# Performance work log

Hardware: AMD Instinct MI355X
Metric: run time of the kernel (lower is better)

The kernel has to match this reference:

```python
import jax, jax.numpy as jnp
import numpy as np

HIDDEN = 1024
INTER = 4096

def setup_inputs() -> dict:
    key = jax.random.key(0)
    k1, k2, k3, k4, k5 = jax.random.split(key, 5)
    hidden_states = jax.random.normal(k1, (4, 2048, HIDDEN), dtype=jnp.float32)
    # Linear params: W stored pre-transposed as [in, out], matching W = dense.weight.t()
    W1 = jax.random.normal(k2, (HIDDEN, INTER), dtype=jnp.float32) * (1.0 / np.sqrt(HIDDEN))
    b1 = jax.random.normal(k3, (INTER,), dtype=jnp.float32) * 0.02
    W2 = jax.random.normal(k4, (INTER, HIDDEN), dtype=jnp.float32) * (1.0 / np.sqrt(INTER))
    b2 = jax.random.normal(k5, (HIDDEN,), dtype=jnp.float32) * 0.02
    return {"hidden_states": hidden_states, "W1": W1, "b1": b1, "W2": W2, "b2": b2}

def reference(hidden_states, W1, b1, W2, b2):
    # Tiled loops in the original are exactly a dense 2-layer MLP with ReLU.
    h = jax.nn.relu(jnp.einsum('bsh,hi->bsi', hidden_states, W1) + b1)
    return jnp.einsum('bsi,ih->bsh', h, W2) + b2
```

## Files before the change

kernel.cpp:

```cpp
#include <hip/hip_runtime.h>
#include <cstddef>

typedef short short8 __attribute__((ext_vector_type(8)));
typedef unsigned short ushort8 __attribute__((ext_vector_type(8)));
typedef float f32x4 __attribute__((ext_vector_type(4)));

#define AS1(p) ((const __attribute__((address_space(1))) void*)(p))
#define AS3(p) ((__attribute__((address_space(3))) void*)(p))

__device__ __forceinline__ unsigned short f2bf(float f) {
  unsigned int u = __builtin_bit_cast(unsigned int, f);
  u += 0x7FFFu + ((u >> 16) & 1u);
  return (unsigned short)(u >> 16);
}

__device__ __forceinline__ void gload_lds16(const void* g, void* l) {
  __builtin_amdgcn_global_load_lds(AS1(g), AS3(l), 16, 0, 0);
}

__global__ __launch_bounds__(256)
void prep_fused(const float* __restrict__ X,
                const float* __restrict__ W1,
                const float* __restrict__ W2,
                unsigned short* __restrict__ Xbf,
                unsigned short* __restrict__ W1t,
                unsigned short* __restrict__ W2t) {
  const int b   = blockIdx.x;
  const int tid = threadIdx.x;

  if (b >= 8192) {
    const size_t i = (size_t)(b - 8192) * 256 + tid;
    float4 v = *reinterpret_cast<const float4*>(X + i * 4);
    ushort4 o;
    o.x = f2bf(v.x); o.y = f2bf(v.y); o.z = f2bf(v.z); o.w = f2bf(v.w);
    *reinterpret_cast<ushort4*>(Xbf + i * 4) = o;
    return;
  }

  __shared__ float tile[32][33];
  const float* in;
  unsigned short* out;
  int Kd, Nd, n0, k0;
  if (b < 4096) {
    in = W1; out = W1t; Kd = 1024; Nd = 4096;
    n0 = (b & 127) * 32;
    k0 = (b >> 7) * 32;
  } else {
    const int b2 = b - 4096;
    in = W2; out = W2t; Kd = 4096; Nd = 1024;
    n0 = (b2 & 31) * 32;
    k0 = (b2 >> 5) * 32;
  }
  const int tx = tid & 31;
  const int ty = tid >> 5;
#pragma unroll
  for (int i = 0; i < 4; ++i)
    tile[ty + i * 8][tx] = in[(size_t)(k0 + ty + i * 8) * Nd + n0 + tx];
  __syncthreads();
#pragma unroll
  for (int i = 0; i < 4; ++i)
    out[(size_t)(n0 + ty + i * 8) * Kd + k0 + tx] = f2bf(tile[tx][ty + i * 8]);
}

__global__ void cvt_f32_bf16(const float* __restrict__ in,
                             unsigned short* __restrict__ out, int n4) {
  int i = blockIdx.x * blockDim.x + threadIdx.x;
  if (i >= n4) return;
  float4 v = *reinterpret_cast<const float4*>(in + (size_t)i * 4);
  ushort4 o;
  o.x = f2bf(v.x); o.y = f2bf(v.y); o.z = f2bf(v.z); o.w = f2bf(v.w);
  *reinterpret_cast<ushort4*>(out + (size_t)i * 4) = o;
}

__global__ void transpose_cvt(const float* __restrict__ in,
                              unsigned short* __restrict__ out,
                              int Kd, int Nd) {
  __shared__ float tile[32][33];
  const int n0 = blockIdx.x * 32;
  const int k0 = blockIdx.y * 32;
  const int tx = threadIdx.x;
  const int ty = threadIdx.y;
#pragma unroll
  for (int i = 0; i < 4; ++i)
    tile[ty + i * 8][tx] = in[(size_t)(k0 + ty + i * 8) * Nd + n0 + tx];
  __syncthreads();
#pragma unroll
  for (int i = 0; i < 4; ++i)
    out[(size_t)(n0 + ty + i * 8) * Kd + k0 + tx] = f2bf(tile[tx][ty + i * 8]);
}

#define PH(ABUF, BBUF, H, KK, STAGE, WAITC)                                    \
  {                                                                            \
    if ((H) == 0) {                                                            \
      _Pragma("unroll")                                                        \
      for (int ni = 0; ni < NB; ++ni)                                          \
        bfr[ni] = *reinterpret_cast<const short8*>((BBUF) + bread[ni][KK]);    \
    }                                                                          \
    short8 afr[4];                                                             \
    _Pragma("unroll")                                                          \
    for (int m2 = 0; m2 < 4; ++m2)                                             \
      afr[m2] = *reinterpret_cast<const short8*>((ABUF) + aread[(H)*4+m2][KK]);\
    STAGE;                                                                     \
    __builtin_amdgcn_s_barrier();                                              \
    asm volatile("s_waitcnt lgkmcnt(0)" ::: "memory");                         \
    __builtin_amdgcn_sched_barrier(0);                                         \
    __builtin_amdgcn_s_setprio(1);                                             \
    _Pragma("unroll")                                                          \
    for (int m2 = 0; m2 < 4; ++m2) {                                           \
      _Pragma("unroll")                                                        \
      for (int ni = 0; ni < NB; ++ni)                                          \
        acc[(H)*4+m2][ni] = __builtin_amdgcn_mfma_f32_16x16x32_bf16(           \
            afr[m2], bfr[ni], acc[(H)*4+m2][ni], 0, 0, 0);                     \
    }                                                                          \
    __builtin_amdgcn_s_setprio(0);                                             \
    WAITC;                                                                     \
    __builtin_amdgcn_s_barrier();                                              \
  }

template <int BN, int RELU_BF16_OUT>
__global__ __launch_bounds__(512, 2)
void gemm8p(const unsigned short* __restrict__ A, int lda,
            const unsigned short* __restrict__ Bp, int ldb,
            const float* __restrict__ bias,
            void* __restrict__ C, int ldc, int K, int nbx) {
  constexpr int PWN     = BN / 4;
  constexpr int NB      = PWN / 16;
  constexpr int LOADS_B = BN / 128;
  constexpr int BHROWS  = BN / 2;
  constexpr int BHSZ    = BHROWS * 128;
  extern __shared__ char lds[];
  char* const A0b = lds;
  char* const A1b = lds + 32768;
  char* const B0b = lds + 65536;
  char* const B1b = lds + 65536 + 2 * BHSZ;

  const int tid  = threadIdx.x;
  const int lane = tid & 63;
  const int wid  = tid >> 6;
  const int wm   = wid >> 2;
  const int wn   = wid & 3;

  const int cpx     = gridDim.x >> 3;
  const int logical = (blockIdx.x & 7) * cpx + (blockIdx.x >> 3);
  const int bx = logical % nbx;
  const int by = logical / nbx;
  const int m0 = by * 256;
  const int n0 = bx * BN;

  f32x4 acc[8][NB];
#pragma unroll
  for (int i = 0; i < 8; ++i)
#pragma unroll
    for (int j = 0; j < NB; ++j)
      acc[i][j] = (f32x4){0.f, 0.f, 0.f, 0.f};

  size_t aofs0, aofs1, bofs0, bofs1 = 0;
  {
    int sr = tid * 16, nat = sr ^ (((sr >> 7) & 7) << 4);
    aofs0 = (size_t)(m0 + (nat >> 7)) * lda + ((nat & 127) >> 1);
    bofs0 = (size_t)(n0 + (nat >> 7)) * ldb + ((nat & 127) >> 1);
    sr = (512 + tid) * 16; nat = sr ^ (((sr >> 7) & 7) << 4);
    aofs1 = (size_t)(m0 + (nat >> 7)) * lda + ((nat & 127) >> 1);
    if (LOADS_B == 2)
      bofs1 = (size_t)(n0 + (nat >> 7)) * ldb + ((nat & 127) >> 1);
  }
  const int dst0 = (tid & 448) * 16;
  const int dst1 = dst0 + 8192;

  auto stA = [&](char* ab, int half, int kel) {
    gload_lds16(A + aofs0 + (size_t)half * 128 * lda + kel, ab + half * 16384 + dst0);
    gload_lds16(A + aofs1 + (size_t)half * 128 * lda + kel, ab + half * 16384 + dst1);
  };
  auto stB = [&](char* bb, int half, int kel) {
    gload_lds16(Bp + bofs0 + (size_t)half * BHROWS * ldb + kel, bb + half * BHSZ + dst0);
    if constexpr (LOADS_B == 2)
      gload_lds16(Bp + bofs1 + (size_t)half * BHROWS * ldb + kel, bb + half * BHSZ + dst1);
  };
  auto waitLB = [&]() {
    if constexpr (LOADS_B == 2) asm volatile("s_waitcnt vmcnt(2)" ::: "memory");
    else                        asm volatile("s_waitcnt vmcnt(1)" ::: "memory");
  };

  int aread[8][2], bread[NB][2];
#pragma unroll
  for (int mi = 0; mi < 8; ++mi)
#pragma unroll
    for (int kk = 0; kk < 2; ++kk) {
      int nat = (wm * 128 + mi * 16 + (lane & 15)) * 128 + kk * 64 + (lane >> 4) * 16;
      aread[mi][kk] = nat ^ (((nat >> 7) & 7) << 4);
    }
#pragma unroll
  for (int ni = 0; ni < NB; ++ni)
#pragma unroll
    for (int kk = 0; kk < 2; ++kk) {
      int nat = (wn * PWN + ni * 16 + (lane & 15)) * 128 + kk * 64 + (lane >> 4) * 16;
      bread[ni][kk] = nat ^ (((nat >> 7) & 7) << 4);
    }

  stB(B0b, 0, 0);
  stB(B0b, 1, 0);
  stA(A0b, 0, 0);
  stA(A0b, 1, 0);
  stB(B1b, 0, 64);
  waitLB();
  __builtin_amdgcn_s_barrier();

  const int niter = K >> 7;
  for (int it = 0; it < niter; ++it) {
    const bool last = (it == niter - 1);
    const int kb = it << 7;
    short8 bfr[NB];
    PH(A0b, B0b, 0, 0, stB(B1b, 1, kb + 64), ((void)0));
    PH(A0b, B0b, 1, 0, stA(A1b, 0, kb + 64), ((void)0));
    PH(A0b, B0b, 0, 1, stA(A1b, 1, kb + 64), ((void)0));
    PH(A0b, B0b, 1, 1, { if (!last) stB(B0b, 0, kb + 128); },
       { if (last) { asm volatile("s_waitcnt vmcnt(0)" ::: "memory"); } else waitLB(); });
    PH(A1b, B1b, 0, 0, { if (!last) stB(B0b, 1, kb + 128); }, ((void)0));
    PH(A1b, B1b, 1, 0, { if (!last) stA(A0b, 0, kb + 128); }, ((void)0));
    PH(A1b, B1b, 0, 1, { if (!last) stA(A0b, 1, kb + 128); }, ((void)0));
    PH(A1b, B1b, 1, 1, { if (!last) stB(B1b, 0, kb + 192); },
       { if (!last) waitLB(); });
  }

  const int row0 = m0 + wm * 128 + (lane >> 4) * 4;
  const int col0 = n0 + wn * PWN + (lane & 15);
#pragma unroll
  for (int ni = 0; ni < NB; ++ni) {
    const int c = col0 + ni * 16;
    const float bv = bias[c];
#pragma unroll
    for (int mi = 0; mi < 8; ++mi) {
#pragma unroll
      for (int r = 0; r < 4; ++r) {
        const size_t idx = (size_t)(row0 + mi * 16 + r) * ldc + c;
        float v = acc[mi][ni][r] + bv;
        if (RELU_BF16_OUT) {
          v = v > 0.f ? v : 0.f;
          ((unsigned short*)C)[idx] = f2bf(v);
        } else {
          ((float*)C)[idx] = v;
        }
      }
    }
  }
}

template <int A_F32, int RELU_BF16_OUT>
__global__ __launch_bounds__(256, 2)
void gemm_bf16(const void* __restrict__ Ap, int lda,
               const unsigned short* __restrict__ B, int ldb,
               const float* __restrict__ bias,
               void* __restrict__ C, int ldc,
               int K, int beta) {
  __shared__ char lds[32768];
  char* const As = lds;
  char* const Bs = lds + 16384;

  const int tid  = threadIdx.x;
  const int lane = tid & 63;
  const int w    = tid >> 6;
  const int wm   = w >> 1;
  const int wn   = w & 1;
  const int m0   = blockIdx.y * 128;
  const int n0   = blockIdx.x * 128;

  f32x4 acc[4][4];
#pragma unroll
  for (int i = 0; i < 4; ++i)
#pragma unroll
    for (int j = 0; j < 4; ++j)
      acc[i][j] = (f32x4){0.f, 0.f, 0.f, 0.f};

  int srow[4], scol[4], sbase[4];
#pragma unroll
  for (int j = 0; j < 4; ++j) {
    const int stored  = (j * 256 + tid) * 16;
    const int natural = stored ^ (((stored >> 7) & 7) << 4);
    srow[j]  = natural >> 7;
    scol[j]  = (natural & 127) >> 1;
    sbase[j] = (j * 256 + (tid & 192)) * 16;
  }

  size_t agofs[4];
  int ast[4];
  if (A_F32) {
#pragma unroll
    for (int pq = 0; pq < 4; ++pq) {
      const int idx = pq * 256 + tid;
      const int rr  = idx >> 3;
      const int kbe = (idx & 7) * 8;
      agofs[pq] = (size_t)(m0 + rr) * lda + kbe;
      const int nat = rr * 128 + kbe * 2;
      ast[pq] = nat ^ (((nat >> 7) & 7) << 4);
    }
  }

  const int nsteps = K >> 6;
  for (int ks = 0; ks < nsteps; ++ks) {
    const int k0 = ks << 6;
    if (A_F32) {
      const float* Af = (const float*)Ap;
#pragma unroll
      for (int pq = 0; pq < 4; ++pq) {
        const float* sp = Af + agofs[pq] + k0;
        float4 x0 = *reinterpret_cast<const float4*>(sp);
        float4 x1 = *reinterpret_cast<const float4*>(sp + 4);
        ushort8 v;
        v[0] = f2bf(x0.x); v[1] = f2bf(x0.y); v[2] = f2bf(x0.z); v[3] = f2bf(x0.w);
        v[4] = f2bf(x1.x); v[5] = f2bf(x1.y); v[6] = f2bf(x1.z); v[7] = f2bf(x1.w);
        *reinterpret_cast<ushort8*>(As + ast[pq]) = v;
      }
    } else {
      const unsigned short* Ab = (const unsigned short*)Ap;
#pragma unroll
      for (int j = 0; j < 4; ++j)
        gload_lds16(Ab + (size_t)(m0 + srow[j]) * lda + (k0 + scol[j]),
                    As + sbase[j]);
    }
#pragma unroll
    for (int j = 0; j < 4; ++j)
      gload_lds16(B + (size_t)(n0 + srow[j]) * ldb + (k0 + scol[j]),
                  Bs + sbase[j]);
    __syncthreads();

#pragma unroll
    for (int kk = 0; kk < 2; ++kk) {
      const int kb = kk * 64 + (lane >> 4) * 16;
      short8 af[4], bfv[4];
#pragma unroll
      for (int mi = 0; mi < 4; ++mi) {
        int nat = (wm * 64 + mi * 16 + (lane & 15)) * 128 + kb;
        int st  = nat ^ (((nat >> 7) & 7) << 4);
        af[mi] = *reinterpret_cast<const short8*>(As + st);
      }
#pragma unroll
      for (int ni = 0; ni < 4; ++ni) {
        int nat = (wn * 64 + ni * 16 + (lane & 15)) * 128 + kb;
        int st  = nat ^ (((nat >> 7) & 7) << 4);
        bfv[ni] = *reinterpret_cast<const short8*>(Bs + st);
      }
#pragma unroll
      for (int mi = 0; mi < 4; ++mi)
#pragma unroll
        for (int ni = 0; ni < 4; ++ni)
          acc[mi][ni] = __builtin_amdgcn_mfma_f32_16x16x32_bf16(
              af[mi], bfv[ni], acc[mi][ni], 0, 0, 0);
    }
    __syncthreads();
  }

  const int row0 = m0 + wm * 64 + (lane >> 4) * 4;
  const int col0 = n0 + wn * 64 + (lane & 15);
#pragma unroll
  for (int ni = 0; ni < 4; ++ni) {
    const int c = col0 + ni * 16;
    const float bv = beta ? 0.f : bias[c];
#pragma unroll
    for (int mi = 0; mi < 4; ++mi) {
#pragma unroll
      for (int rr = 0; rr < 4; ++rr) {
        const size_t idx = (size_t)(row0 + mi * 16 + rr) * ldc + c;
        float v = acc[mi][ni][rr] + bv;
        if (RELU_BF16_OUT) {
          v = v > 0.f ? v : 0.f;
          ((unsigned short*)C)[idx] = f2bf(v);
        } else {
          if (beta) v += ((float*)C)[idx];
          ((float*)C)[idx] = v;
        }
      }
    }
  }
}

extern "C" void kernel_launch(void* const* d_in, const int* in_sizes, int n_in,
                              void* d_out, int out_size, void* d_ws, size_t ws_size,
                              hipStream_t stream) {
  const float* X  = (const float*)d_in[0];
  const float* W1 = (const float*)d_in[1];
  const float* b1 = (const float*)d_in[2];
  const float* W2 = (const float*)d_in[3];
  const float* b2 = (const float*)d_in[4];
  float* out = (float*)d_out;

  const int M = 8192, H = 1024, I = 4096;
  const size_t MB = 1024 * 1024;

  char* ws = (char*)d_ws;
  unsigned short* W1t = (unsigned short*)ws;
  unsigned short* W2t = (unsigned short*)(ws + 8 * MB);

  if (ws_size >= 80 * MB) {
    unsigned short* Xbf = (unsigned short*)((char*)d_out + 16 * MB);
    unsigned short* Hbf = (unsigned short*)(ws + 16 * MB);
    prep_fused<<<16384, 256, 0, stream>>>(X, W1, W2, Xbf, W1t, W2t);
    gemm8p<256, 1><<<512, 512, 131072, stream>>>(Xbf, H, W1t, H, b1, Hbf, I, H, I / 256);
    gemm8p<128, 0><<<256, 512, 98304, stream>>>(Hbf, I, W2t, I, b2, out, H, I, H / 128);
    return;
  }

  transpose_cvt<<<dim3(I / 32, H / 32), dim3(32, 8), 0, stream>>>(W1, W1t, H, I);
  transpose_cvt<<<dim3(H / 32, I / 32), dim3(32, 8), 0, stream>>>(W2, W2t, I, H);

  int Ic, useXbf;
  unsigned short* Xbf = nullptr;
  unsigned short* Hc;
  if (ws_size >= 64 * MB) {
    Ic = 2048; useXbf = 1;
    Xbf = (unsigned short*)(ws + 16 * MB);
    Hc  = (unsigned short*)(ws + 32 * MB);
  } else if (ws_size >= 48 * MB) {
    Ic = 1024; useXbf = 1;
    Xbf = (unsigned short*)(ws + 16 * MB);
    Hc  = (unsigned short*)(ws + 32 * MB);
  } else if (ws_size >= 32 * MB) {
    Ic = 1024; useXbf = 0;
    Hc  = (unsigned short*)(ws + 16 * MB);
  } else if (ws_size >= 24 * MB) {
    Ic = 512;  useXbf = 0;
    Hc  = (unsigned short*)(ws + 16 * MB);
  } else if (ws_size >= 20 * MB) {
    Ic = 256;  useXbf = 0;
    Hc  = (unsigned short*)(ws + 16 * MB);
  } else {
    Ic = 128;  useXbf = 0;
    Hc  = (unsigned short*)(ws + 16 * MB);
  }

  if (useXbf) {
    int n4 = (M * H) / 4;
    cvt_f32_bf16<<<(n4 + 255) / 256, 256, 0, stream>>>(X, Xbf, n4);
  }

  const int nch = I / Ic;
  for (int c = 0; c < nch; ++c) {
    const int i0 = c * Ic;
    if (useXbf)
      gemm_bf16<0, 1><<<dim3(Ic / 128, M / 128), 256, 0, stream>>>(
          Xbf, H, W1t + (size_t)i0 * H, H, b1 + i0, Hc, Ic, H, 0);
    else
      gemm_bf16<1, 1><<<dim3(Ic / 128, M / 128), 256, 0, stream>>>(
          X, H, W1t + (size_t)i0 * H, H, b1 + i0, Hc, Ic, H, 0);
    gemm_bf16<0, 0><<<dim3(H / 128, M / 128), 256, 0, stream>>>(
        Hc, Ic, W2t + i0, I, b2, out, H, Ic, c > 0);
  }
}
```

Before: 161.7 us.

## Replace first GEMM with 256-thread 256x256-tile double-buffered bf16 MFMA kernel

Adds a new GEMM kernel, gemm_bw, for the first MLP layer. Each 4-wave workgroup computes a 256x256 tile with an 8x8 grid of 16x16x32 MFMA accumulators per wave. It uses double-buffered global-to-LDS loads into an XOR-swizzled layout and a simple vmcnt wait and barrier pipeline. It replaces the 512-thread gemm8p variant to cut per-wave LDS reads and scheduling overhead. The cost is very high register pressure (256 accumulator VGPRs) and a simpler pipeline with less fine-grained overlap.

```diff
diff --git a/kernel.cpp b/kernel.cpp
--- a/kernel.cpp
+++ b/kernel.cpp
@@ -16,6 +16,11 @@
 
 __device__ __forceinline__ void gload_lds16(const void* g, void* l) {
   __builtin_amdgcn_global_load_lds(AS1(g), AS3(l), 16, 0, 0);
+}
+
+template <int N>
+__device__ __forceinline__ void vwait() {
+  asm volatile("s_waitcnt vmcnt(%0)" :: "n"(N) : "memory");
 }
 
 __global__ __launch_bounds__(256)
@@ -87,6 +92,130 @@
 #pragma unroll
   for (int i = 0; i < 4; ++i)
     out[(size_t)(n0 + ty + i * 8) * Kd + k0 + tx] = f2bf(tile[tx][ty + i * 8]);
+}
+
+template <int RELU_BF16_OUT>
+__global__ __launch_bounds__(256, 1)
+void gemm_bw(const unsigned short* __restrict__ A, int lda,
+             const unsigned short* __restrict__ B, int ldb,
+             const float* __restrict__ bias,
+             void* __restrict__ C, int ldc, int K, int nbx) {
+  extern __shared__ char lds[];
+
+  const int tid  = threadIdx.x;
+  const int lane = tid & 63;
+  const int wid  = tid >> 6;
+  const int wm   = wid >> 1;
+  const int wn   = wid & 1;
+
+  const int cpx     = gridDim.x >> 3;
+  const int logical = (blockIdx.x & 7) * cpx + (blockIdx.x >> 3);
+  const int m0 = (logical / nbx) * 256;
+  const int n0 = (logical % nbx) * 256;
+
+  f32x4 acc[8][8];
+#pragma unroll
+  for (int i = 0; i < 8; ++i)
+#pragma unroll
+    for (int j = 0; j < 8; ++j)
+      acc[i][j] = (f32x4){0.f, 0.f, 0.f, 0.f};
+
+  size_t aofs[8], bofs[8];
+  int sb[8];
+#pragma unroll
+  for (int j = 0; j < 8; ++j) {
+    const int stored = (j * 256 + tid) * 16;
+    const int nat    = stored ^ (((stored >> 7) & 7) << 4);
+    const int row    = nat >> 7;
+    const int kel    = (nat & 127) >> 1;
+    aofs[j] = (size_t)(m0 + row) * lda + kel;
+    bofs[j] = (size_t)(n0 + row) * ldb + kel;
+    sb[j]   = j * 4096 + (tid & 192) * 16;
+  }
+
+  auto stage = [&](int d, int k0) {
+    char* ab = lds + d * 65536;
+    char* bb = ab + 32768;
+#pragma unroll
+    for (int j = 0; j < 8; ++j) gload_lds16(A + aofs[j] + k0, ab + sb[j]);
+#pragma unroll
+    for (int j = 0; j < 8; ++j) gload_lds16(B + bofs[j] + k0, bb + sb[j]);
+  };
+
+  int ard[8][2], brd[8][2];
+#pragma unroll
+  for (int mi = 0; mi < 8; ++mi)
+#pragma unroll
+    for (int kk = 0; kk < 2; ++kk) {
+      const int nat = (wm * 128 + mi * 16 + (lane & 15)) * 128 +
+                      kk * 64 + (lane >> 4) * 16;
+      ard[mi][kk] = nat ^ (((nat >> 7) & 7) << 4);
+    }
+#pragma unroll
+  for (int ni = 0; ni < 8; ++ni)
+#pragma unroll
+    for (int kk = 0; kk < 2; ++kk) {
+      const int nat = (wn * 128 + ni * 16 + (lane & 15)) * 128 +
+                      kk * 64 + (lane >> 4) * 16;
+      brd[ni][kk] = nat ^ (((nat >> 7) & 7) << 4);
+    }
+
+  stage(0, 0);
+
+  const int NT = K >> 6;
+  for (int t = 0; t < NT; ++t) {
+    const int cur = t & 1;
+    if (t + 1 < NT) {
+      stage(cur ^ 1, (t + 1) << 6);
+      vwait<16>();
+    } else {
+      vwait<0>();
+    }
+    __builtin_amdgcn_s_barrier();
+    __builtin_amdgcn_sched_barrier(0);
+
+    char* ab = lds + cur * 65536;
+    char* bb = ab + 32768;
+#pragma unroll
+    for (int kk = 0; kk < 2; ++kk) {
+      short8 bfv[8];
+#pragma unroll
+      for (int ni = 0; ni < 8; ++ni)
+        bfv[ni] = *reinterpret_cast<const short8*>(bb + brd[ni][kk]);
+#pragma unroll
+      for (int mi = 0; mi < 8; ++mi) {
+        const short8 af = *reinterpret_cast<const short8*>(ab + ard[mi][kk]);
+#pragma unroll
+        for (int ni = 0; ni < 8; ++ni)
+          acc[mi][ni] = __builtin_amdgcn_mfma_f32_16x16x32_bf16(
+              af, bfv[ni], acc[mi][ni], 0, 0, 0);
+      }
+    }
+    __builtin_amdgcn_sched_barrier(0);
+    __builtin_amdgcn_s_barrier();
+  }
+
+  const int row0 = m0 + wm * 128 + (lane >> 4) * 4;
+  const int col0 = n0 + wn * 128 + (lane & 15);
+#pragma unroll
+  for (int ni = 0; ni < 8; ++ni) {
+    const int c = col0 + ni * 16;
+    const float bv = bias[c];
+#pragma unroll
+    for (int mi = 0; mi < 8; ++mi) {
+#pragma unroll
+      for (int r = 0; r < 4; ++r) {
+        const size_t idx = (size_t)(row0 + mi * 16 + r) * ldc + c;
+        float v = acc[mi][ni][r] + bv;
+        if (RELU_BF16_OUT) {
+          v = v > 0.f ? v : 0.f;
+          ((unsigned short*)C)[idx] = f2bf(v);
+        } else {
+          ((float*)C)[idx] = v;
+        }
+      }
+    }
+  }
 }
 
 #define PH(ABUF, BBUF, H, KK, STAGE, WAITC)                                    \
@@ -394,8 +523,10 @@
     unsigned short* Xbf = (unsigned short*)((char*)d_out + 16 * MB);
     unsigned short* Hbf = (unsigned short*)(ws + 16 * MB);
     prep_fused<<<16384, 256, 0, stream>>>(X, W1, W2, Xbf, W1t, W2t);
-    gemm8p<256, 1><<<512, 512, 131072, stream>>>(Xbf, H, W1t, H, b1, Hbf, I, H, I / 256);
-    gemm8p<128, 0><<<256, 512, 98304, stream>>>(Hbf, I, W2t, I, b2, out, H, I, H / 128);
+    gemm_bw<1><<<512, 256, 131072, stream>>>(
+        Xbf, H, W1t, H, b1, Hbf, I, H, I / 256);
+    gemm8p<128, 0><<<256, 512, 98304, stream>>>(
+        Hbf, I, W2t, I, b2, out, H, I, H / 128);
     return;
   }
 
```

After: 211.3 us. 30.7% more time.

## Replace 8-phase interleaved GEMM pipeline with simple double-buffered K=64 loop

Applied to the files above, without the earlier changes.

Swaps the hand-scheduled 8-phase ping-pong GEMM, which interleaved partial A/B loads with MFMA groups and used setprio and sched barriers, for a plain double-buffered loop. Each step issues the whole next 64-wide K tile into the other LDS buffer, waits for the previous tile, and runs all MFMAs on it. This makes the schedule simpler and needs fewer barriers per step. It risks losing the fine-grained overlap and wave-priority tuning of the old pipeline.

```diff
diff --git a/kernel.cpp b/kernel.cpp
--- a/kernel.cpp
+++ b/kernel.cpp
@@ -16,6 +16,11 @@
 
 __device__ __forceinline__ void gload_lds16(const void* g, void* l) {
   __builtin_amdgcn_global_load_lds(AS1(g), AS3(l), 16, 0, 0);
+}
+
+template <int N>
+__device__ __forceinline__ void vwait() {
+  asm volatile("s_waitcnt vmcnt(%0)" :: "n"(N) : "memory");
 }
 
 __global__ __launch_bounds__(256)
@@ -89,50 +94,19 @@
     out[(size_t)(n0 + ty + i * 8) * Kd + k0 + tx] = f2bf(tile[tx][ty + i * 8]);
 }
 
-#define PH(ABUF, BBUF, H, KK, STAGE, WAITC)                                    \
-  {                                                                            \
-    if ((H) == 0) {                                                            \
-      _Pragma("unroll")                                                        \
-      for (int ni = 0; ni < NB; ++ni)                                          \
-        bfr[ni] = *reinterpret_cast<const short8*>((BBUF) + bread[ni][KK]);    \
-    }                                                                          \
-    short8 afr[4];                                                             \
-    _Pragma("unroll")                                                          \
-    for (int m2 = 0; m2 < 4; ++m2)                                             \
-      afr[m2] = *reinterpret_cast<const short8*>((ABUF) + aread[(H)*4+m2][KK]);\
-    STAGE;                                                                     \
-    __builtin_amdgcn_s_barrier();                                              \
-    asm volatile("s_waitcnt lgkmcnt(0)" ::: "memory");                         \
-    __builtin_amdgcn_sched_barrier(0);                                         \
-    __builtin_amdgcn_s_setprio(1);                                             \
-    _Pragma("unroll")                                                          \
-    for (int m2 = 0; m2 < 4; ++m2) {                                           \
-      _Pragma("unroll")                                                        \
-      for (int ni = 0; ni < NB; ++ni)                                          \
-        acc[(H)*4+m2][ni] = __builtin_amdgcn_mfma_f32_16x16x32_bf16(           \
-            afr[m2], bfr[ni], acc[(H)*4+m2][ni], 0, 0, 0);                     \
-    }                                                                          \
-    __builtin_amdgcn_s_setprio(0);                                             \
-    WAITC;                                                                     \
-    __builtin_amdgcn_s_barrier();                                              \
-  }
-
 template <int BN, int RELU_BF16_OUT>
 __global__ __launch_bounds__(512, 2)
-void gemm8p(const unsigned short* __restrict__ A, int lda,
-            const unsigned short* __restrict__ Bp, int ldb,
-            const float* __restrict__ bias,
-            void* __restrict__ C, int ldc, int K, int nbx) {
-  constexpr int PWN     = BN / 4;
-  constexpr int NB      = PWN / 16;
-  constexpr int LOADS_B = BN / 128;
-  constexpr int BHROWS  = BN / 2;
-  constexpr int BHSZ    = BHROWS * 128;
+void gemm_cf(const unsigned short* __restrict__ A, int lda,
+             const unsigned short* __restrict__ B, int ldb,
+             const float* __restrict__ bias,
+             void* __restrict__ C, int ldc, int K, int nbx) {
+  constexpr int PWN    = BN / 4;
+  constexpr int NB     = PWN / 16;
+  constexpr int AUNITS = 4;
+  constexpr int BUNITS = BN / 64;
+  constexpr int LPT    = AUNITS + BUNITS;
+  constexpr int BUFSZ  = 32768 + BN * 128;
   extern __shared__ char lds[];
-  char* const A0b = lds;
-  char* const A1b = lds + 32768;
-  char* const B0b = lds + 65536;
-  char* const B1b = lds + 65536 + 2 * BHSZ;
 
   const int tid  = threadIdx.x;
   const int lane = tid & 63;
@@ -142,10 +116,8 @@
 
   const int cpx     = gridDim.x >> 3;
   const int logical = (blockIdx.x & 7) * cpx + (blockIdx.x >> 3);
-  const int bx = logical % nbx;
-  const int by = logical / nbx;
-  const int m0 = by * 256;
-  const int n0 = bx * BN;
+  const int m0 = (logical / nbx) * 256;
+  const int n0 = (logical % nbx) * BN;
 
   f32x4 acc[8][NB];
 #pragma unroll
@@ -154,72 +126,80 @@
     for (int j = 0; j < NB; ++j)
       acc[i][j] = (f32x4){0.f, 0.f, 0.f, 0.f};
 
-  size_t aofs0, aofs1, bofs0, bofs1 = 0;
-  {
-    int sr = tid * 16, nat = sr ^ (((sr >> 7) & 7) << 4);
-    aofs0 = (size_t)(m0 + (nat >> 7)) * lda + ((nat & 127) >> 1);
-    bofs0 = (size_t)(n0 + (nat >> 7)) * ldb + ((nat & 127) >> 1);
-    sr = (512 + tid) * 16; nat = sr ^ (((sr >> 7) & 7) << 4);
-    aofs1 = (size_t)(m0 + (nat >> 7)) * lda + ((nat & 127) >> 1);
-    if (LOADS_B == 2)
-      bofs1 = (size_t)(n0 + (nat >> 7)) * ldb + ((nat & 127) >> 1);
-  }
-  const int dst0 = (tid & 448) * 16;
-  const int dst1 = dst0 + 8192;
-
-  auto stA = [&](char* ab, int half, int kel) {
-    gload_lds16(A + aofs0 + (size_t)half * 128 * lda + kel, ab + half * 16384 + dst0);
-    gload_lds16(A + aofs1 + (size_t)half * 128 * lda + kel, ab + half * 16384 + dst1);
+  size_t aofs[AUNITS], bofs[BUNITS];
+  const int ldst = (tid & 448) * 16;
+#pragma unroll
+  for (int u = 0; u < AUNITS; ++u) {
+    const int s   = (u * 512 + tid) * 16;
+    const int nat = s ^ (((s >> 7) & 7) << 4);
+    aofs[u] = (size_t)(m0 + (nat >> 7)) * lda + ((nat & 127) >> 1);
+  }
+#pragma unroll
+  for (int u = 0; u < BUNITS; ++u) {
+    const int s   = (u * 512 + tid) * 16;
+    const int nat = s ^ (((s >> 7) & 7) << 4);
+    bofs[u] = (size_t)(n0 + (nat >> 7)) * ldb + ((nat & 127) >> 1);
+  }
+
+  auto stage = [&](int d, int k0) {
+    char* ab = lds + d * BUFSZ;
+    char* bb = ab + 32768;
+#pragma unroll
+    for (int u = 0; u < AUNITS; ++u)
+      gload_lds16(A + aofs[u] + k0, ab + u * 8192 + ldst);
+#pragma unroll
+    for (int u = 0; u < BUNITS; ++u)
+      gload_lds16(B + bofs[u] + k0, bb + u * 8192 + ldst);
   };
-  auto stB = [&](char* bb, int half, int kel) {
-    gload_lds16(Bp + bofs0 + (size_t)half * BHROWS * ldb + kel, bb + half * BHSZ + dst0);
-    if constexpr (LOADS_B == 2)
-      gload_lds16(Bp + bofs1 + (size_t)half * BHROWS * ldb + kel, bb + half * BHSZ + dst1);
-  };
-  auto waitLB = [&]() {
-    if constexpr (LOADS_B == 2) asm volatile("s_waitcnt vmcnt(2)" ::: "memory");
-    else                        asm volatile("s_waitcnt vmcnt(1)" ::: "memory");
-  };
-
-  int aread[8][2], bread[NB][2];
+
+  int ard[8][2], brd[NB][2];
 #pragma unroll
   for (int mi = 0; mi < 8; ++mi)
 #pragma unroll
     for (int kk = 0; kk < 2; ++kk) {
-      int nat = (wm * 128 + mi * 16 + (lane & 15)) * 128 + kk * 64 + (lane >> 4) * 16;
-      aread[mi][kk] = nat ^ (((nat >> 7) & 7) << 4);
+      const int nat = (wm * 128 + mi * 16 + (lane & 15)) * 128 +
+                      kk * 64 + (lane >> 4) * 16;
+      ard[mi][kk] = nat ^ (((nat >> 7) & 7) << 4);
     }
 #pragma unroll
   for (int ni = 0; ni < NB; ++ni)
 #pragma unroll
     for (int kk = 0; kk < 2; ++kk) {
-      int nat = (wn * PWN + ni * 16 + (lane & 15)) * 128 + kk * 64 + (lane >> 4) * 16;
-      bread[ni][kk] = nat ^ (((nat >> 7) & 7) << 4);
-    }
-
-  stB(B0b, 0, 0);
-  stB(B0b, 1, 0);
-  stA(A0b, 0, 0);
-  stA(A0b, 1, 0);
-  stB(B1b, 0, 64);
-  waitLB();
-  __builtin_amdgcn_s_barrier();
-
-  const int niter = K >> 7;
-  for (int it = 0; it < niter; ++it) {
-    const bool last = (it == niter - 1);
-    const int kb = it << 7;
-    short8 bfr[NB];
-    PH(A0b, B0b, 0, 0, stB(B1b, 1, kb + 64), ((void)0));
-    PH(A0b, B0b, 1, 0, stA(A1b, 0, kb + 64), ((void)0));
-    PH(A0b, B0b, 0, 1, stA(A1b, 1, kb + 64), ((void)0));
-    PH(A0b, B0b, 1, 1, { if (!last) stB(B0b, 0, kb + 128); },
-       { if (last) { asm volatile("s_waitcnt vmcnt(0)" ::: "memory"); } else waitLB(); });
-    PH(A1b, B1b, 0, 0, { if (!last) stB(B0b, 1, kb + 128); }, ((void)0));
-    PH(A1b, B1b, 1, 0, { if (!last) stA(A0b, 0, kb + 128); }, ((void)0));
-    PH(A1b, B1b, 0, 1, { if (!last) stA(A0b, 1, kb + 128); }, ((void)0));
-    PH(A1b, B1b, 1, 1, { if (!last) stB(B1b, 0, kb + 192); },
-       { if (!last) waitLB(); });
+      const int nat = (wn * PWN + ni * 16 + (lane & 15)) * 128 +
+                      kk * 64 + (lane >> 4) * 16;
+      brd[ni][kk] = 32768 + (nat ^ (((nat >> 7) & 7) << 4));
+    }
+
+  stage(0, 0);
+
+  const int NT = K >> 6;
+  for (int t = 0; t < NT; ++t) {
+    const int cur = t & 1;
+    if (t + 1 < NT) {
+      stage(cur ^ 1, (t + 1) << 6);
+      vwait<LPT>();
+    } else {
+      vwait<0>();
+    }
+    __builtin_amdgcn_s_barrier();
+
+    char* ab = lds + cur * BUFSZ;
+#pragma unroll
+    for (int kk = 0; kk < 2; ++kk) {
+      short8 bfv[NB];
+#pragma unroll
+      for (int ni = 0; ni < NB; ++ni)
+        bfv[ni] = *reinterpret_cast<const short8*>(ab + brd[ni][kk]);
+#pragma unroll
+      for (int mi = 0; mi < 8; ++mi) {
+        const short8 af = *reinterpret_cast<const short8*>(ab + ard[mi][kk]);
+#pragma unroll
+        for (int ni = 0; ni < NB; ++ni)
+          acc[mi][ni] = __builtin_amdgcn_mfma_f32_16x16x32_bf16(
+              af, bfv[ni], acc[mi][ni], 0, 0, 0);
+      }
+    }
+    __builtin_amdgcn_s_barrier();
   }
 
   const int row0 = m0 + wm * 128 + (lane >> 4) * 4;
@@ -394,8 +374,10 @@
     unsigned short* Xbf = (unsigned short*)((char*)d_out + 16 * MB);
     unsigned short* Hbf = (unsigned short*)(ws + 16 * MB);
     prep_fused<<<16384, 256, 0, stream>>>(X, W1, W2, Xbf, W1t, W2t);
-    gemm8p<256, 1><<<512, 512, 131072, stream>>>(Xbf, H, W1t, H, b1, Hbf, I, H, I / 256);
-    gemm8p<128, 0><<<256, 512, 98304, stream>>>(Hbf, I, W2t, I, b2, out, H, I, H / 128);
+    gemm_cf<256, 1><<<512, 512, 131072, stream>>>(
+        Xbf, H, W1t, H, b1, Hbf, I, H, I / 256);
+    gemm_cf<128, 0><<<256, 512, 98304, stream>>>(
+        Hbf, I, W2t, I, b2, out, H, I, H / 128);
     return;
   }
 
```

Measured after the change: 165.8 us. +2.5%, slower.
